# Kernel tuning notes

Measured on AMD Instinct MI355X. Metric: run time of the kernel, lower is better.

Reference implementation:

```python
import jax, jax.numpy as jnp
import numpy as np

HAD_BLOCK = 128
HAD_SCALE = 2.0 ** (-3.5)  # 1/sqrt(128), orthonormal block Hadamard


def _hadamard_matrix(n):
    H = np.array([[1.0]], dtype=np.float32)
    while H.shape[0] < n:
        H = np.block([[H, H], [H, -H]])
    return jnp.asarray(H)

_H = _hadamard_matrix(HAD_BLOCK)


def hadamard_transform(x, scale):
    # x: (..., D) with D % 128 == 0; blockwise Hadamard rotation on last dim
    shp = x.shape
    xb = x.reshape(shp[:-1] + (shp[-1] // HAD_BLOCK, HAD_BLOCK))
    y = jnp.einsum('...b,cb->...c', xb, _H) * scale
    return y.reshape(shp)


def setup_inputs() -> dict:
    key = jax.random.key(0)
    kx, kw, kb = jax.random.split(key, 3)
    B, S, IN, OUT = 4, 2048, 4096, 4096
    x = jax.random.normal(kx, (B, S, IN), dtype=jnp.float32)
    # master fp weight, then preprocess: Hadamard-rotate rows, quantize to int4,
    # pack two nibbles per element (per-out-channel scale/add)
    w = jax.random.normal(kw, (OUT, IN), dtype=jnp.float32) / np.float32(np.sqrt(IN))
    w_had = hadamard_transform(w, HAD_SCALE)
    wmin = w_had.min(axis=1, keepdims=True)
    wmax = w_had.max(axis=1, keepdims=True)
    w_scale = jnp.maximum((wmax - wmin) / 15.0, 1e-8)  # [OUT,1]
    w_add = wmin                                        # [OUT,1]
    w_int = jnp.clip(jnp.round((w_had - w_add) / w_scale), 0, 15).astype(jnp.int32)
    w_int_packed = (w_int[:, ::2] | (w_int[:, 1::2] << 4)).astype(jnp.int32)  # [OUT, IN//2]
    bias = jax.random.normal(kb, (OUT,), dtype=jnp.float32) * 0.01
    return {"x": x, "w_int_packed": w_int_packed, "w_scale": w_scale,
            "w_add": w_add, "bias": bias}


def reference(x, w_int_packed, w_scale, w_add, bias):
    OUT = w_int_packed.shape[0]
    IN = w_int_packed.shape[1] * 2
    # unpack int4 nibbles -> [OUT, IN]
    low = w_int_packed & 0xF
    high = (w_int_packed >> 4) & 0xF
    w_int = jnp.stack([low, high], axis=-1).reshape(OUT, IN).astype(w_scale.dtype)
    # per-out-channel dequant
    w_deq = w_int * w_scale + w_add  # [OUT, IN]
    # fused Hadamard rotation on activations (matches rotated weight)
    a = hadamard_transform(x, HAD_SCALE)  # [B,S,IN]
    y = jnp.einsum('bsi,oi->bso', a, w_deq)
    return y + bias
```

## Files before the change

### kernel.cpp

```cpp
#include <hip/hip_runtime.h>
#include <hip/hip_bf16.h>
#include <hip/hip_fp16.h>

#define IN_DIM 4096
#define OUT_DIM 4096
#define HAD_SCALE_F 0.08838834764831845f

typedef int   i32x4 __attribute__((ext_vector_type(4)));
typedef float f32x4 __attribute__((ext_vector_type(4)));

__global__ __launch_bounds__(256)
void had_rows_q(const float* __restrict__ x, int* __restrict__ aq,
                float* __restrict__ rowsum, float* __restrict__ srow)
{
    __shared__ float wmx[4];
    __shared__ int   wqs[4];
    const int tid = threadIdx.x;
    const int wv  = tid >> 6;
    const size_t row = blockIdx.x;
    const float* xr = x + row * IN_DIM + tid * 16;

    float e[16];
    #pragma unroll
    for (int v = 0; v < 4; ++v) {
        const float4 f = ((const float4*)xr)[v];
        e[v*4+0] = f.x; e[v*4+1] = f.y; e[v*4+2] = f.z; e[v*4+3] = f.w;
    }

    #pragma unroll
    for (int s = 1; s < 16; s <<= 1) {
        #pragma unroll
        for (int i = 0; i < 16; ++i) {
            if (!(i & s)) {
                const float u = e[i], w2 = e[i | s];
                e[i]     = u + w2;
                e[i | s] = u - w2;
            }
        }
    }
    #pragma unroll
    for (int m = 1; m <= 4; m <<= 1) {
        const float sgn = (tid & m) ? -1.0f : 1.0f;
        #pragma unroll
        for (int i = 0; i < 16; ++i) {
            const float p = __shfl_xor(e[i], m, 64);
            e[i] = fmaf(sgn, e[i], p);
        }
    }

    float smax = 0.f;
    #pragma unroll
    for (int i = 0; i < 16; ++i) {
        e[i] *= HAD_SCALE_F;
        smax = fmaxf(smax, fabsf(e[i]));
    }
    #pragma unroll
    for (int off = 32; off > 0; off >>= 1)
        smax = fmaxf(smax, __shfl_xor(smax, off, 64));
    if ((tid & 63) == 0) wmx[wv] = smax;
    __syncthreads();
    const float mx  = fmaxf(fmaxf(wmx[0], wmx[1]), fmaxf(wmx[2], wmx[3]));
    const float inv = (mx > 0.f) ? 127.0f / mx : 0.f;
    const float sa  = mx * (1.0f / 127.0f);

    int qsum = 0;
    int pk[4];
    #pragma unroll
    for (int g2 = 0; g2 < 4; ++g2) {
        const int q0 = (int)rintf(e[g2*4+0] * inv);
        const int q1 = (int)rintf(e[g2*4+1] * inv);
        const int q2 = (int)rintf(e[g2*4+2] * inv);
        const int q3 = (int)rintf(e[g2*4+3] * inv);
        qsum += (q0 + q1) + (q2 + q3);
        pk[g2] = (q0 & 0xFF) | ((q1 & 0xFF) << 8) | ((q2 & 0xFF) << 16) | (q3 << 24);
    }
    *(int4*)&aq[row * (IN_DIM / 4) + tid * 4] = make_int4(pk[0], pk[1], pk[2], pk[3]);

    #pragma unroll
    for (int off = 32; off > 0; off >>= 1) qsum += __shfl_xor(qsum, off, 64);
    if ((tid & 63) == 0) wqs[wv] = qsum;
    __syncthreads();
    if (tid == 0) {
        rowsum[row] = sa * (float)((wqs[0] + wqs[1]) + (wqs[2] + wqs[3]));
        srow[row]   = sa;
    }
}

__global__ __launch_bounds__(256)
void unpack_w8(const int* __restrict__ wp, signed char* __restrict__ wf8)
{
    const int gid = blockIdx.x * 256 + threadIdx.x;
    const int n   = gid >> 9;
    const int k0  = (gid & 511) * 8;
    const int4 p  = *(const int4*)(wp + (size_t)n * (IN_DIM / 2) + (k0 >> 1));
    const unsigned lo = (unsigned)(p.x & 15) | ((unsigned)((p.x >> 4) & 15) << 8)
                      | ((unsigned)(p.y & 15) << 16) | ((unsigned)((p.y >> 4) & 15) << 24);
    const unsigned hi = (unsigned)(p.z & 15) | ((unsigned)((p.z >> 4) & 15) << 8)
                      | ((unsigned)(p.w & 15) << 16) | ((unsigned)((p.w >> 4) & 15) << 24);
    *(uint2*)(wf8 + (size_t)n * IN_DIM + k0) = make_uint2(lo, hi);
}

#define NT (IN_DIM / 128)
#define NI (NT / 2)

#define BAR()        asm volatile("s_barrier" ::: "memory")
#define WAIT_VM(N)   asm volatile("s_waitcnt vmcnt(" #N ")" ::: "memory")

#define STAGE_A(p, R, kt) __builtin_amdgcn_global_load_lds( \
    (const __attribute__((address_space(1))) void*)(sA + (((size_t)(R)) << 18) + (((size_t)((kt) & 31)) << 7)), \
    (__attribute__((address_space(3))) void*)(smem + (p) * 65536 + (R) * 8192 + dstA), 16, 0, 0)
#define STAGE_B(p, R, kt) __builtin_amdgcn_global_load_lds( \
    (const __attribute__((address_space(1))) void*)(sB + (((size_t)(R)) << 18) + (((size_t)((kt) & 31)) << 7)), \
    (__attribute__((address_space(3))) void*)(smem + (p) * 65536 + (R) * 8192 + dstB), 16, 0, 0)

#define LDA(p, mq, mi, kb) (*(const i32x4*)(smem + (p)*65536 + (mq)*8192 + (mi)*2048 + aOffK[kb]))
#define LDB(p, nq, ni, kb) (*(const i32x4*)(smem + (p)*65536 + (nq)*4096 + (ni)*2048 + bOffK[kb]))

#define LOAD_A_TO(dst, p, mq) do { \
    _Pragma("unroll") for (int mi = 0; mi < 4; ++mi) { \
        dst[mi][0] = LDA(p, mq, mi, 0); \
        dst[mi][1] = LDA(p, mq, mi, 1); \
    } } while (0)

#define LOAD_B(p, nq) do { \
    _Pragma("unroll") for (int ni = 0; ni < 2; ++ni) { \
        bfr[(nq)*2+ni][0] = LDB(p, nq, ni, 0); \
        bfr[(nq)*2+ni][1] = LDB(p, nq, ni, 1); \
    } } while (0)

#define MFMA_Q(abuf, mq, nq) do { \
    __builtin_amdgcn_s_setprio(1); \
    _Pragma("unroll") for (int kb = 0; kb < 2; ++kb) \
    _Pragma("unroll") for (int mi = 0; mi < 4; ++mi) \
    _Pragma("unroll") for (int ni = 0; ni < 2; ++ni) \
        acc[(mq)*4+mi][(nq)*2+ni] = __builtin_amdgcn_mfma_i32_16x16x64_i8( \
            abuf[mi][kb], bfr[(nq)*2+ni][kb], acc[(mq)*4+mi][(nq)*2+ni], 0, 0, 0); \
    __builtin_amdgcn_s_setprio(0); \
} while (0)

__global__ __launch_bounds__(512, 2)
void gemm_i8(const signed char* __restrict__ Aq, const signed char* __restrict__ Bw,
             const float* __restrict__ wscale, const float* __restrict__ wadd,
             const float* __restrict__ bias, const float* __restrict__ rowsum,
             const float* __restrict__ srow, float* __restrict__ out)
{
    __shared__ char smem[131072];

    const int tid  = threadIdx.x;
    const int lane = tid & 63;
    const int w    = tid >> 6;
    const int wm   = w >> 2;
    const int wn   = w & 3;

    const int bid = blockIdx.x;
    const int wg  = (bid & 7) * 64 + (bid >> 3);
    const int m0  = (wg >> 4) * 256;
    const int n0  = (wg & 15) * 256;

    const int rt = tid >> 3;
    const int ct = (tid & 7) ^ (rt & 7);
    const signed char* sA = Aq + (size_t)(m0 + rt) * IN_DIM + ct * 16;
    const signed char* sB = Bw + (size_t)(n0 + rt) * IN_DIM + ct * 16;
    const int dstA = w * 1024;
    const int dstB = 32768 + w * 1024;

    const int l15 = lane & 15, g = lane >> 4, l7 = lane & 7;
    const int s0 = (g ^ l7) << 4;
    int aOffK[2], bOffK[2];
    aOffK[0] = (wm * 128 + l15) * 128 + s0;
    aOffK[1] = (wm * 128 + l15) * 128 + (s0 ^ 64);
    bOffK[0] = 32768 + (wn * 64 + l15) * 128 + s0;
    bOffK[1] = 32768 + (wn * 64 + l15) * 128 + (s0 ^ 64);

    i32x4 afrA[4][2], afrB[4][2], bfr[4][2];
    i32x4 acc[8][4] = {};

    #pragma unroll
    for (int R = 0; R < 4; ++R) { STAGE_A(0, R, 0); STAGE_B(0, R, 0); }
    #pragma unroll
    for (int R = 0; R < 4; ++R) { STAGE_A(1, R, 1); STAGE_B(1, R, 1); }
    WAIT_VM(8);
    BAR();
    LOAD_B(0, 0);
    LOAD_A_TO(afrA, 0, 0);

    #pragma unroll 1
    for (int it = 0; it < NI; ++it) {
        const int kt1 = 2 * it + 1;
        const int kt2 = (2 * it + 2) & (NT - 1);
        const int kt3 = (2 * it + 3) & (NT - 1);

        LOAD_B(0, 1);
        if (it) { STAGE_B(1, 2, kt1); STAGE_B(1, 3, kt1);
                  STAGE_A(1, 1, kt1); STAGE_A(1, 3, kt1); }
        MFMA_Q(afrA, 0, 0);
        LOAD_A_TO(afrB, 0, 1);
        MFMA_Q(afrA, 0, 1);
        if (it) { WAIT_VM(2); } else { WAIT_VM(0); }
        BAR();

        STAGE_B(0, 0, kt2); STAGE_B(0, 1, kt2);
        MFMA_Q(afrB, 1, 0);
        LOAD_B(1, 0);
        LOAD_A_TO(afrA, 1, 0);
        STAGE_A(0, 0, kt2); STAGE_A(0, 2, kt2);
        MFMA_Q(afrB, 1, 1);
        WAIT_VM(4);
        BAR();

        STAGE_B(0, 2, kt2); STAGE_B(0, 3, kt2);
        MFMA_Q(afrA, 0, 0);
        LOAD_B(1, 1);
        LOAD_A_TO(afrB, 1, 1);
        STAGE_A(0, 1, kt2); STAGE_A(0, 3, kt2);
        MFMA_Q(afrA, 0, 1);
        WAIT_VM(2);
        BAR();

        STAGE_B(1, 0, kt3); STAGE_B(1, 1, kt3);
        MFMA_Q(afrB, 1, 0);
        LOAD_B(0, 0);
        LOAD_A_TO(afrA, 0, 0);
        STAGE_A(1, 0, kt3); STAGE_A(1, 2, kt3);
        MFMA_Q(afrB, 1, 1);
        WAIT_VM(4);
        BAR();
    }

    #pragma unroll
    for (int n = 0; n < 4; ++n) {
        const int col = n0 + wn * 64 + n * 16 + l15;
        const float sc = wscale[col];
        const float ad = wadd[col];
        const float bi = bias[col];
        #pragma unroll
        for (int m = 0; m < 8; ++m) {
            const int row = m0 + wm * 128 + m * 16 + g * 4;
            const float4 rs4 = *(const float4*)&rowsum[row];
            const float4 sr4 = *(const float4*)&srow[row];
            #pragma unroll
            for (int j = 0; j < 4; ++j) {
                const float rs = (j == 0) ? rs4.x : (j == 1) ? rs4.y : (j == 2) ? rs4.z : rs4.w;
                const float sr = (j == 0) ? sr4.x : (j == 1) ? sr4.y : (j == 2) ? sr4.z : sr4.w;
                out[(size_t)(row + j) * OUT_DIM + col] =
                    (float)acc[m][n][j] * (sc * sr) + ad * rs + bi;
            }
        }
    }
}

extern "C" void kernel_launch(void* const* d_in, const int* in_sizes, int n_in,
                              void* d_out, int out_size, void* d_ws, size_t ws_size,
                              hipStream_t stream)
{
    const float* x      = (const float*)d_in[0];
    const int*   wp     = (const int*)d_in[1];
    const float* wscale = (const float*)d_in[2];
    const float* wadd   = (const float*)d_in[3];
    const float* bias   = (const float*)d_in[4];
    float*       out    = (float*)d_out;

    const int M = in_sizes[0] / IN_DIM;

    char* ws = (char*)d_ws;
    signed char* wf8 = (signed char*)ws;
    const size_t wf_bytes = (size_t)OUT_DIM * IN_DIM;
    int* aq = (int*)(ws + wf_bytes);
    const size_t aq_bytes = (size_t)M * IN_DIM;
    float* rowsum = (float*)(ws + wf_bytes + aq_bytes);
    float* srow   = (float*)(ws + wf_bytes + aq_bytes + (size_t)M * 4);

    const int unpack_blocks = (OUT_DIM * (IN_DIM / 8)) / 256;
    unpack_w8<<<unpack_blocks, 256, 0, stream>>>(wp, wf8);

    had_rows_q<<<M, 256, 0, stream>>>(x, aq, rowsum, srow);

    gemm_i8<<<(M / 256) * (OUT_DIM / 256), 512, 0, stream>>>(
        (const signed char*)aq, wf8, wscale, wadd, bias, rowsum, srow, out);
}
```

Measured before the change: 181.3 us.

## Keep weights int4-packed in GEMM and unpack nibbles in registers

The weight preprocessing now repacks int4 weights into a nibble-interleaved layout at half the size of the former int8 expansion. The GEMM loads these packed tiles into LDS and splits them into low and high nibbles in registers before issuing int8 MFMAs. This halves weight traffic and LDS footprint. The tile also shrinks to 128x256 with 256 threads and a simpler single-step double-buffered pipeline, which adds VALU unpack work per k-step and a less overlapped schedule than the previous hand-tuned one.

```diff
diff --git a/kernel.cpp b/kernel.cpp
--- a/kernel.cpp
+++ b/kernel.cpp
@@ -87,155 +87,166 @@
 }
 
 __global__ __launch_bounds__(256)
-void unpack_w8(const int* __restrict__ wp, signed char* __restrict__ wf8)
+void unpack_w4i(const int* __restrict__ wp, unsigned char* __restrict__ wf4)
 {
     const int gid = blockIdx.x * 256 + threadIdx.x;
-    const int n   = gid >> 9;
-    const int k0  = (gid & 511) * 8;
-    const int4 p  = *(const int4*)(wp + (size_t)n * (IN_DIM / 2) + (k0 >> 1));
-    const unsigned lo = (unsigned)(p.x & 15) | ((unsigned)((p.x >> 4) & 15) << 8)
-                      | ((unsigned)(p.y & 15) << 16) | ((unsigned)((p.y >> 4) & 15) << 24);
-    const unsigned hi = (unsigned)(p.z & 15) | ((unsigned)((p.z >> 4) & 15) << 8)
-                      | ((unsigned)(p.w & 15) << 16) | ((unsigned)((p.w >> 4) & 15) << 24);
-    *(uint2*)(wf8 + (size_t)n * IN_DIM + k0) = make_uint2(lo, hi);
-}
-
-#define NT (IN_DIM / 128)
-#define NI (NT / 2)
+    const int c   = gid & 3;
+    const int kt  = (gid >> 2) & 31;
+    const int n   = gid >> 7;
+    const int kbase = kt * 128 + c * 16;
+    const int* row = wp + (size_t)n * (IN_DIM / 2) + (kbase >> 1);
+    const int4 plo0 = *(const int4*)(row);
+    const int4 plo1 = *(const int4*)(row + 4);
+    const int4 phi0 = *(const int4*)(row + 32);
+    const int4 phi1 = *(const int4*)(row + 36);
+
+    #define MKD(lo, hi, lo2, hi2) \
+        ( (unsigned)(((lo) & 15) | (((hi) & 15) << 4)) \
+        | ((unsigned)((((lo) >> 4) & 15) | ((((hi) >> 4) & 15) << 4)) << 8) \
+        | ((unsigned)(((lo2) & 15) | (((hi2) & 15) << 4)) << 16) \
+        | ((unsigned)((((lo2) >> 4) & 15) | ((((hi2) >> 4) & 15) << 4)) << 24) )
+
+    uint4 o;
+    o.x = MKD(plo0.x, phi0.x, plo0.y, phi0.y);
+    o.y = MKD(plo0.z, phi0.z, plo0.w, phi0.w);
+    o.z = MKD(plo1.x, phi1.x, plo1.y, phi1.y);
+    o.w = MKD(plo1.z, phi1.z, plo1.w, phi1.w);
+    #undef MKD
+    *(uint4*)(wf4 + (size_t)gid * 16) = o;
+}
+
+#define NT 32
 
 #define BAR()        asm volatile("s_barrier" ::: "memory")
 #define WAIT_VM(N)   asm volatile("s_waitcnt vmcnt(" #N ")" ::: "memory")
-
-#define STAGE_A(p, R, kt) __builtin_amdgcn_global_load_lds( \
-    (const __attribute__((address_space(1))) void*)(sA + (((size_t)(R)) << 18) + (((size_t)((kt) & 31)) << 7)), \
-    (__attribute__((address_space(3))) void*)(smem + (p) * 65536 + (R) * 8192 + dstA), 16, 0, 0)
-#define STAGE_B(p, R, kt) __builtin_amdgcn_global_load_lds( \
-    (const __attribute__((address_space(1))) void*)(sB + (((size_t)(R)) << 18) + (((size_t)((kt) & 31)) << 7)), \
-    (__attribute__((address_space(3))) void*)(smem + (p) * 65536 + (R) * 8192 + dstB), 16, 0, 0)
-
-#define LDA(p, mq, mi, kb) (*(const i32x4*)(smem + (p)*65536 + (mq)*8192 + (mi)*2048 + aOffK[kb]))
-#define LDB(p, nq, ni, kb) (*(const i32x4*)(smem + (p)*65536 + (nq)*4096 + (ni)*2048 + bOffK[kb]))
-
-#define LOAD_A_TO(dst, p, mq) do { \
-    _Pragma("unroll") for (int mi = 0; mi < 4; ++mi) { \
-        dst[mi][0] = LDA(p, mq, mi, 0); \
-        dst[mi][1] = LDA(p, mq, mi, 1); \
-    } } while (0)
-
-#define LOAD_B(p, nq) do { \
-    _Pragma("unroll") for (int ni = 0; ni < 2; ++ni) { \
-        bfr[(nq)*2+ni][0] = LDB(p, nq, ni, 0); \
-        bfr[(nq)*2+ni][1] = LDB(p, nq, ni, 1); \
-    } } while (0)
-
-#define MFMA_Q(abuf, mq, nq) do { \
-    __builtin_amdgcn_s_setprio(1); \
-    _Pragma("unroll") for (int kb = 0; kb < 2; ++kb) \
-    _Pragma("unroll") for (int mi = 0; mi < 4; ++mi) \
-    _Pragma("unroll") for (int ni = 0; ni < 2; ++ni) \
-        acc[(mq)*4+mi][(nq)*2+ni] = __builtin_amdgcn_mfma_i32_16x16x64_i8( \
-            abuf[mi][kb], bfr[(nq)*2+ni][kb], acc[(mq)*4+mi][(nq)*2+ni], 0, 0, 0); \
-    __builtin_amdgcn_s_setprio(0); \
-} while (0)
-
-__global__ __launch_bounds__(512, 2)
-void gemm_i8(const signed char* __restrict__ Aq, const signed char* __restrict__ Bw,
+#define WAIT_LGKM0() asm volatile("s_waitcnt lgkmcnt(0)" ::: "memory")
+
+#define STAGE_A(buf, kt) do { \
+    _Pragma("unroll") for (int R = 0; R < 4; ++R) \
+        __builtin_amdgcn_global_load_lds( \
+            (const __attribute__((address_space(1))) void*)(sA + ((size_t)R << 17) + (((kt) & 31) << 7)), \
+            (__attribute__((address_space(3))) void*)(smem + (buf) * 16384 + R * 4096 + wv * 1024), 16, 0, 0); \
+    } while (0)
+#define STAGE_B(kt) do { \
+    _Pragma("unroll") for (int R = 0; R < 4; ++R) \
+        __builtin_amdgcn_global_load_lds( \
+            (const __attribute__((address_space(1))) void*)(sB + ((size_t)R << 17) + (((kt) & 31) << 6)), \
+            (__attribute__((address_space(3))) void*)(smem + 32768 + R * 4096 + wv * 1024), 16, 0, 0); \
+    } while (0)
+
+__global__ __launch_bounds__(256, 2)
+void gemm_i8(const signed char* __restrict__ Aq, const unsigned char* __restrict__ Bw4,
              const float* __restrict__ wscale, const float* __restrict__ wadd,
              const float* __restrict__ bias, const float* __restrict__ rowsum,
              const float* __restrict__ srow, float* __restrict__ out)
 {
-    __shared__ char smem[131072];
+    __shared__ char smem[49152];
 
     const int tid  = threadIdx.x;
     const int lane = tid & 63;
-    const int w    = tid >> 6;
-    const int wm   = w >> 2;
-    const int wn   = w & 3;
+    const int wv   = tid >> 6;
 
     const int bid = blockIdx.x;
-    const int wg  = (bid & 7) * 64 + (bid >> 3);
-    const int m0  = (wg >> 4) * 256;
+    const int wg  = (bid & 7) * 128 + (bid >> 3);
+    const int m0  = (wg >> 4) * 128;
     const int n0  = (wg & 15) * 256;
 
-    const int rt = tid >> 3;
-    const int ct = (tid & 7) ^ (rt & 7);
-    const signed char* sA = Aq + (size_t)(m0 + rt) * IN_DIM + ct * 16;
-    const signed char* sB = Bw + (size_t)(n0 + rt) * IN_DIM + ct * 16;
-    const int dstA = w * 1024;
-    const int dstB = 32768 + w * 1024;
-
-    const int l15 = lane & 15, g = lane >> 4, l7 = lane & 7;
-    const int s0 = (g ^ l7) << 4;
-    int aOffK[2], bOffK[2];
-    aOffK[0] = (wm * 128 + l15) * 128 + s0;
-    aOffK[1] = (wm * 128 + l15) * 128 + (s0 ^ 64);
-    bOffK[0] = 32768 + (wn * 64 + l15) * 128 + s0;
-    bOffK[1] = 32768 + (wn * 64 + l15) * 128 + (s0 ^ 64);
-
-    i32x4 afrA[4][2], afrB[4][2], bfr[4][2];
+    const int art = tid >> 3;
+    const int act = (tid & 7) ^ (art & 7);
+    const signed char* sA = Aq + (size_t)(m0 + art) * IN_DIM + act * 16;
+
+    const int brt = tid >> 2;
+    const int bct = (tid & 3) ^ (brt & 3);
+    const unsigned char* sB = Bw4 + (size_t)(n0 + brt) * 2048 + bct * 16;
+
+    const int l15 = lane & 15, g = lane >> 4, l7 = lane & 7, l3 = lane & 3;
+    const int aOff = l15 * 128 + ((g ^ l7) << 4);
+    const int bOff = 32768 + (wv * 64 + l15) * 64 + ((g ^ l3) << 4);
+
+    i32x4 afr[4][2], b0[4], b1[4];
     i32x4 acc[8][4] = {};
 
-    #pragma unroll
-    for (int R = 0; R < 4; ++R) { STAGE_A(0, R, 0); STAGE_B(0, R, 0); }
-    #pragma unroll
-    for (int R = 0; R < 4; ++R) { STAGE_A(1, R, 1); STAGE_B(1, R, 1); }
-    WAIT_VM(8);
+    STAGE_A(0, 0);
+    STAGE_B(0);
+    WAIT_VM(0);
     BAR();
-    LOAD_B(0, 0);
-    LOAD_A_TO(afrA, 0, 0);
 
     #pragma unroll 1
-    for (int it = 0; it < NI; ++it) {
-        const int kt1 = 2 * it + 1;
-        const int kt2 = (2 * it + 2) & (NT - 1);
-        const int kt3 = (2 * it + 3) & (NT - 1);
-
-        LOAD_B(0, 1);
-        if (it) { STAGE_B(1, 2, kt1); STAGE_B(1, 3, kt1);
-                  STAGE_A(1, 1, kt1); STAGE_A(1, 3, kt1); }
-        MFMA_Q(afrA, 0, 0);
-        LOAD_A_TO(afrB, 0, 1);
-        MFMA_Q(afrA, 0, 1);
-        if (it) { WAIT_VM(2); } else { WAIT_VM(0); }
+    for (int kt = 0; kt < NT; ++kt) {
+        const int cur = kt & 1;
+
+        STAGE_A(cur ^ 1, kt + 1);
+
+        i32x4 bp[4];
+        #pragma unroll
+        for (int ni = 0; ni < 4; ++ni)
+            bp[ni] = *(const i32x4*)(smem + bOff + ni * 1024);
+        #pragma unroll
+        for (int mi = 0; mi < 4; ++mi) {
+            afr[mi][0] = *(const i32x4*)(smem + cur * 16384 + mi * 2048 + aOff);
+            afr[mi][1] = *(const i32x4*)(smem + cur * 16384 + mi * 2048 + (aOff ^ 64));
+        }
+        #pragma unroll
+        for (int ni = 0; ni < 4; ++ni) {
+            #pragma unroll
+            for (int d = 0; d < 4; ++d) {
+                b0[ni][d] = bp[ni][d] & 0x0F0F0F0F;
+                b1[ni][d] = (int)(((unsigned)bp[ni][d] >> 4) & 0x0F0F0F0F);
+            }
+        }
+
+        WAIT_LGKM0();
         BAR();
-
-        STAGE_B(0, 0, kt2); STAGE_B(0, 1, kt2);
-        MFMA_Q(afrB, 1, 0);
-        LOAD_B(1, 0);
-        LOAD_A_TO(afrA, 1, 0);
-        STAGE_A(0, 0, kt2); STAGE_A(0, 2, kt2);
-        MFMA_Q(afrB, 1, 1);
-        WAIT_VM(4);
+        STAGE_B(kt + 1);
+
+        __builtin_amdgcn_s_setprio(1);
+        #pragma unroll
+        for (int mi = 0; mi < 4; ++mi)
+            #pragma unroll
+            for (int ni = 0; ni < 4; ++ni)
+                acc[mi][ni] = __builtin_amdgcn_mfma_i32_16x16x64_i8(
+                    afr[mi][0], b0[ni], acc[mi][ni], 0, 0, 0);
+        #pragma unroll
+        for (int mi = 0; mi < 4; ++mi)
+            #pragma unroll
+            for (int ni = 0; ni < 4; ++ni)
+                acc[mi][ni] = __builtin_amdgcn_mfma_i32_16x16x64_i8(
+                    afr[mi][1], b1[ni], acc[mi][ni], 0, 0, 0);
+        __builtin_amdgcn_s_setprio(0);
+
+        #pragma unroll
+        for (int mi = 0; mi < 4; ++mi) {
+            afr[mi][0] = *(const i32x4*)(smem + cur * 16384 + (mi + 4) * 2048 + aOff);
+            afr[mi][1] = *(const i32x4*)(smem + cur * 16384 + (mi + 4) * 2048 + (aOff ^ 64));
+        }
+        __builtin_amdgcn_s_setprio(1);
+        #pragma unroll
+        for (int mi = 0; mi < 4; ++mi)
+            #pragma unroll
+            for (int ni = 0; ni < 4; ++ni)
+                acc[mi + 4][ni] = __builtin_amdgcn_mfma_i32_16x16x64_i8(
+                    afr[mi][0], b0[ni], acc[mi + 4][ni], 0, 0, 0);
+        #pragma unroll
+        for (int mi = 0; mi < 4; ++mi)
+            #pragma unroll
+            for (int ni = 0; ni < 4; ++ni)
+                acc[mi + 4][ni] = __builtin_amdgcn_mfma_i32_16x16x64_i8(
+                    afr[mi][1], b1[ni], acc[mi + 4][ni], 0, 0, 0);
+        __builtin_amdgcn_s_setprio(0);
+
+        WAIT_VM(0);
         BAR();
-
-        STAGE_B(0, 2, kt2); STAGE_B(0, 3, kt2);
-        MFMA_Q(afrA, 0, 0);
-        LOAD_B(1, 1);
-        LOAD_A_TO(afrB, 1, 1);
-        STAGE_A(0, 1, kt2); STAGE_A(0, 3, kt2);
-        MFMA_Q(afrA, 0, 1);
-        WAIT_VM(2);
-        BAR();
-
-        STAGE_B(1, 0, kt3); STAGE_B(1, 1, kt3);
-        MFMA_Q(afrB, 1, 0);
-        LOAD_B(0, 0);
-        LOAD_A_TO(afrA, 0, 0);
-        STAGE_A(1, 0, kt3); STAGE_A(1, 2, kt3);
-        MFMA_Q(afrB, 1, 1);
-        WAIT_VM(4);
-        BAR();
-    }
-
-    #pragma unroll
-    for (int n = 0; n < 4; ++n) {
-        const int col = n0 + wn * 64 + n * 16 + l15;
+    }
+
+    #pragma unroll
+    for (int ni = 0; ni < 4; ++ni) {
+        const int col = n0 + wv * 64 + ni * 16 + l15;
         const float sc = wscale[col];
         const float ad = wadd[col];
         const float bi = bias[col];
         #pragma unroll
-        for (int m = 0; m < 8; ++m) {
-            const int row = m0 + wm * 128 + m * 16 + g * 4;
+        for (int mi = 0; mi < 8; ++mi) {
+            const int row = m0 + mi * 16 + g * 4;
             const float4 rs4 = *(const float4*)&rowsum[row];
             const float4 sr4 = *(const float4*)&srow[row];
             #pragma unroll
@@ -243,7 +254,7 @@
                 const float rs = (j == 0) ? rs4.x : (j == 1) ? rs4.y : (j == 2) ? rs4.z : rs4.w;
                 const float sr = (j == 0) ? sr4.x : (j == 1) ? sr4.y : (j == 2) ? sr4.z : sr4.w;
                 out[(size_t)(row + j) * OUT_DIM + col] =
-                    (float)acc[m][n][j] * (sc * sr) + ad * rs + bi;
+                    (float)acc[mi][ni][j] * (sc * sr) + ad * rs + bi;
             }
         }
     }
@@ -263,18 +274,17 @@
     const int M = in_sizes[0] / IN_DIM;
 
     char* ws = (char*)d_ws;
-    signed char* wf8 = (signed char*)ws;
-    const size_t wf_bytes = (size_t)OUT_DIM * IN_DIM;
+    unsigned char* wf4 = (unsigned char*)ws;
+    const size_t wf_bytes = (size_t)OUT_DIM * IN_DIM / 2;
     int* aq = (int*)(ws + wf_bytes);
     const size_t aq_bytes = (size_t)M * IN_DIM;
     float* rowsum = (float*)(ws + wf_bytes + aq_bytes);
     float* srow   = (float*)(ws + wf_bytes + aq_bytes + (size_t)M * 4);
 
-    const int unpack_blocks = (OUT_DIM * (IN_DIM / 8)) / 256;
-    unpack_w8<<<unpack_blocks, 256, 0, stream>>>(wp, wf8);
+    unpack_w4i<<<(OUT_DIM * 32 * 4) / 256, 256, 0, stream>>>(wp, wf4);
 
     had_rows_q<<<M, 256, 0, stream>>>(x, aq, rowsum, srow);
 
-    gemm_i8<<<(M / 256) * (OUT_DIM / 256), 512, 0, stream>>>(
-        (const signed char*)aq, wf8, wscale, wadd, bias, rowsum, srow, out);
-}
+    gemm_i8<<<(M / 128) * (OUT_DIM / 256), 256, 0, stream>>>(
+        (const signed char*)aq, wf4, wscale, wadd, bias, rowsum, srow, out);
+}
```

After: 175.0 us, median of 2. 3.5% less time.
